# Kernel tuning notes

Hardware: AMD Instinct MI355X
Metric: run time of the kernel (lower is better)

The kernel has to match this reference:

```python
import jax, jax.numpy as jnp
import numpy as np

N_EMB = 1024
HEAD_SIZE = 128

def setup_inputs() -> dict:
    key = jax.random.key(0)
    kx, kq, kk, kv = jax.random.split(key, 4)
    s = 1.0 / np.sqrt(N_EMB)
    return {
        "x": jax.random.normal(kx, (4, 4096, N_EMB), dtype=jnp.float32),
        "Wq": jax.random.normal(kq, (N_EMB, HEAD_SIZE), dtype=jnp.float32) * s,
        "Wk": jax.random.normal(kk, (N_EMB, HEAD_SIZE), dtype=jnp.float32) * s,
        "Wv": jax.random.normal(kv, (N_EMB, HEAD_SIZE), dtype=jnp.float32) * s,
    }

def reference(x, Wq, Wk, Wv) -> jnp.ndarray:
    B, T, C = x.shape
    q = jnp.einsum('btc,cd->btd', x, Wq)  # [B,T,H]
    k = jnp.einsum('btc,cd->btd', x, Wk)
    v = jnp.einsum('btc,cd->btd', x, Wv)
    # NOTE: original scales by sqrt(n_emb), not sqrt(head_size)
    wei = jnp.einsum('btd,bsd->bts', q, k) / jnp.sqrt(jnp.asarray(C, x.dtype))
    causal = jnp.tril(jnp.ones((T, T), dtype=bool))
    wei = jnp.where(causal, wei, -jnp.inf)
    wei = jax.nn.softmax(wei, axis=-1)
    return jnp.einsum('bts,bsd->btd', wei, v)
```

## Files before the change

kernel.cpp:

```cpp
#include <hip/hip_runtime.h>
#include <hip/hip_bf16.h>


#define TSEQ 4096
#define NBATCH 4
#define CEMB 1024
#define HS 128
#define NWORK 272

typedef float  f32x4  __attribute__((ext_vector_type(4)));
typedef float  f32x16 __attribute__((ext_vector_type(16)));
typedef __bf16 bf16x4 __attribute__((ext_vector_type(4)));
typedef __bf16 bf16x8 __attribute__((ext_vector_type(8)));
typedef int    i32x2  __attribute__((ext_vector_type(2)));
typedef int    i32x4  __attribute__((ext_vector_type(4)));

__device__ __forceinline__ __bf16 f2b(float f) { return (__bf16)f; }
__device__ __forceinline__ float fexp2(float f) { return __builtin_amdgcn_exp2f(f); }

__global__ void wtrans_kernel(const float* __restrict__ Wq,
                              const float* __restrict__ Wk,
                              const float* __restrict__ Wv,
                              __bf16* __restrict__ Wt) {
  const float* W = (blockIdx.y == 0) ? Wq : (blockIdx.y == 1) ? Wk : Wv;
  int g  = blockIdx.x * 256 + threadIdx.x;
  int n  = g & 127;
  int k0 = (g >> 7) * 8;
  bf16x8 v;
#pragma unroll
  for (int i = 0; i < 8; ++i) v[i] = f2b(W[(size_t)(k0 + i) * HS + n]);
  *(bf16x8*)(Wt + (size_t)blockIdx.y * HS * CEMB + (size_t)n * CEMB + k0) = v;
}

__global__ __launch_bounds__(128)
void proj_kernel(const float* __restrict__ x, const __bf16* __restrict__ Wt,
                 __bf16* __restrict__ qb, __bf16* __restrict__ kb,
                 __bf16* __restrict__ vt) {
  __shared__ __align__(16) __bf16 As[64 * 72];
  __shared__ __align__(16) __bf16 Bs[128 * 72];

  const int tid  = threadIdx.x;
  const int lane = tid & 63;
  const int w    = tid >> 6;
  const int l31  = lane & 31;
  const int half = lane >> 5;

  const int bid   = blockIdx.x;
  const int xcd   = bid & 7;
  const int rest  = bid >> 3;
  const int mat   = rest % 3;
  const int mslab = rest / 3;
  const int m0    = (xcd + 8 * mslab) * 64;
  const __bf16* Wm = Wt + (size_t)mat * HS * CEMB;

  f32x16 acc[2][2];
#pragma unroll
  for (int a = 0; a < 2; ++a)
#pragma unroll
    for (int b = 0; b < 2; ++b)
#pragma unroll
      for (int r = 0; r < 16; ++r) acc[a][b][r] = 0.f;

  const int srow = tid >> 3;
  const int soff = tid & 7;

  f32x4  pa[4][2];
  bf16x8 pb[8];
#pragma unroll
  for (int i = 0; i < 4; ++i) {
    const float* p = x + (size_t)(m0 + srow + 16 * i) * CEMB + soff * 8;
    pa[i][0] = *(const f32x4*)p;
    pa[i][1] = *(const f32x4*)(p + 4);
  }
#pragma unroll
  for (int i = 0; i < 8; ++i)
    pb[i] = *(const bf16x8*)(Wm + (size_t)(srow + 16 * i) * CEMB + soff * 8);

  for (int ks = 0; ks < CEMB; ks += 64) {
    __syncthreads();
#pragma unroll
    for (int i = 0; i < 4; ++i) {
      bf16x8 h;
#pragma unroll
      for (int j = 0; j < 4; ++j) {
        h[j]     = f2b(pa[i][0][j]);
        h[4 + j] = f2b(pa[i][1][j]);
      }
      *(bf16x8*)(As + (srow + 16 * i) * 72 + soff * 8) = h;
    }
#pragma unroll
    for (int i = 0; i < 8; ++i)
      *(bf16x8*)(Bs + (srow + 16 * i) * 72 + soff * 8) = pb[i];
    __syncthreads();
    if (ks + 64 < CEMB) {
#pragma unroll
      for (int i = 0; i < 4; ++i) {
        const float* p = x + (size_t)(m0 + srow + 16 * i) * CEMB + ks + 64 + soff * 8;
        pa[i][0] = *(const f32x4*)p;
        pa[i][1] = *(const f32x4*)(p + 4);
      }
#pragma unroll
      for (int i = 0; i < 8; ++i)
        pb[i] = *(const bf16x8*)(Wm + (size_t)(srow + 16 * i) * CEMB + ks + 64 + soff * 8);
    }
#pragma unroll
    for (int kc = 0; kc < 4; ++kc) {
      bf16x8 af[2], bf[2];
#pragma unroll
      for (int mi = 0; mi < 2; ++mi)
        af[mi] = *(const bf16x8*)(As + (mi * 32 + l31) * 72 + kc * 16 + half * 8);
#pragma unroll
      for (int ni = 0; ni < 2; ++ni)
        bf[ni] = *(const bf16x8*)(Bs + (64 * w + ni * 32 + l31) * 72 + kc * 16 + half * 8);
#pragma unroll
      for (int mi = 0; mi < 2; ++mi)
#pragma unroll
        for (int ni = 0; ni < 2; ++ni)
          acc[mi][ni] = __builtin_amdgcn_mfma_f32_32x32x16_bf16(
              af[mi], bf[ni], acc[mi][ni], 0, 0, 0);
    }
  }

  const float qscale = 1.4426950408889634f / 32.0f;
  if (mat == 0) {
#pragma unroll
    for (int mi = 0; mi < 2; ++mi)
#pragma unroll
      for (int ni = 0; ni < 2; ++ni) {
        int n = 64 * w + ni * 32 + l31;
#pragma unroll
        for (int r = 0; r < 16; ++r) {
          int m = m0 + mi * 32 + (r & 3) + 8 * (r >> 2) + 4 * half;
          qb[(size_t)m * HS + n] = f2b(acc[mi][ni][r] * qscale);
        }
      }
  } else if (mat == 1) {
#pragma unroll
    for (int mi = 0; mi < 2; ++mi)
#pragma unroll
      for (int ni = 0; ni < 2; ++ni) {
        int n = 64 * w + ni * 32 + l31;
#pragma unroll
        for (int r = 0; r < 16; ++r) {
          int m = m0 + mi * 32 + (r & 3) + 8 * (r >> 2) + 4 * half;
          kb[(size_t)m * HS + n] = f2b(acc[mi][ni][r]);
        }
      }
  } else {
    const int bt = m0 >> 12;
#pragma unroll
    for (int mi = 0; mi < 2; ++mi)
#pragma unroll
      for (int ni = 0; ni < 2; ++ni) {
        int n = 64 * w + ni * 32 + l31;
#pragma unroll
        for (int g = 0; g < 4; ++g) {
          bf16x4 pk;
#pragma unroll
          for (int d = 0; d < 4; ++d) pk[d] = f2b(acc[mi][ni][4 * g + d]);
          int tl = ((m0 + mi * 32) & 4095) + 8 * g + 4 * half;
          *(bf16x4*)(vt + ((size_t)bt * HS + n) * TSEQ + tl) = pk;
        }
      }
  }
}

__global__ __launch_bounds__(256)
void attn_kernel(const __bf16* __restrict__ qb, const __bf16* __restrict__ kb,
                 const __bf16* __restrict__ vt,
                 __bf16* __restrict__ Opart, float* __restrict__ Lpart) {
  __shared__ __align__(16) __bf16 Kt[64 * 136];
  __shared__ __align__(16) __bf16 Vtl[128 * 72];

  const int tid   = threadIdx.x;
  const int lane  = tid & 63;
  const int w     = tid >> 6;
  const int l31   = lane & 31;
  const int half  = lane >> 5;
  const int batch = blockIdx.y;
  const int xw    = blockIdx.x;

  int q = 0;
  while (q < 31 && xw >= (((q + 2) * (q + 2)) >> 2)) ++q;
  const int split = xw - (((q + 1) * (q + 1)) >> 2);
  const int ntile = 2 * (q + 1);
  const int nsp   = (q + 2) >> 1;
  const int tps   = (ntile + nsp - 1) / nsp;
  const int it0   = split * tps;
  const int it1   = min(it0 + tps, ntile);

  const int strip0 = q * 128 + w * 32;
  const size_t bbase = (size_t)batch * TSEQ;

  bf16x8 qf[8];
  {
    const __bf16* qr = qb + (bbase + strip0 + l31) * HS + half * 8;
#pragma unroll
    for (int kc = 0; kc < 8; ++kc) qf[kc] = *(const bf16x8*)(qr + kc * 16);
  }

  const __bf16* kbb = kb + bbase * HS;
  const __bf16* vbb = vt + (size_t)batch * HS * TSEQ;

  bf16x8 pkr[4], pvr[4];
  {
    const int c0 = it0 * 64;
#pragma unroll
    for (int i = 0; i < 4; ++i) {
      int c = tid + i * 256;
      pkr[i] = *(const bf16x8*)(kbb + (size_t)(c0 + (c >> 4)) * HS + (c & 15) * 8);
      pvr[i] = *(const bf16x8*)(vbb + (size_t)(c >> 3) * TSEQ + c0 + (c & 7) * 8);
    }
  }

  f32x16 o[4];
#pragma unroll
  for (int nt = 0; nt < 4; ++nt)
#pragma unroll
    for (int r = 0; r < 16; ++r) o[nt][r] = 0.f;
  float lsum = 0.f;

  for (int it = it0; it < it1; ++it) {
    const int c0 = it * 64;
    __syncthreads();
#pragma unroll
    for (int i = 0; i < 4; ++i) {
      int c = tid + i * 256;
      *(bf16x8*)(&Kt[(c >> 4) * 136 + (c & 15) * 8]) = pkr[i];
      *(bf16x8*)(&Vtl[(c >> 3) * 72 + (c & 7) * 8]) = pvr[i];
    }
    __syncthreads();
    if (it + 1 < it1) {
      const int c1 = c0 + 64;
#pragma unroll
      for (int i = 0; i < 4; ++i) {
        int c = tid + i * 256;
        pkr[i] = *(const bf16x8*)(kbb + (size_t)(c1 + (c >> 4)) * HS + (c & 15) * 8);
        pvr[i] = *(const bf16x8*)(vbb + (size_t)(c >> 3) * TSEQ + c1 + (c & 7) * 8);
      }
    }

    if (c0 <= strip0 + 31) {
      i32x2 pkt[2][4];
#pragma unroll
      for (int t = 0; t < 2; ++t)
#pragma unroll
        for (int j = 0; j < 4; ++j) pkt[t][j] = (i32x2){0, 0};

#pragma unroll
      for (int t = 0; t < 2; ++t) {
        if (c0 + t * 32 <= strip0 + 31) {
          f32x16 s;
#pragma unroll
          for (int r = 0; r < 16; ++r) s[r] = 0.f;
          __builtin_amdgcn_s_setprio(1);
#pragma unroll
          for (int kc = 0; kc < 8; ++kc) {
            bf16x8 kf = *(const bf16x8*)(&Kt[(t * 32 + l31) * 136 + kc * 16 + half * 8]);
            s = __builtin_amdgcn_mfma_f32_32x32x16_bf16(kf, qf[kc], s, 0, 0, 0);
          }
          __builtin_amdgcn_s_setprio(0);
          if (c0 + t * 32 + 31 > strip0) {
#pragma unroll
            for (int r = 0; r < 16; ++r) {
              int key = c0 + t * 32 + (r & 3) + 8 * (r >> 2) + 4 * half;
              if (key > strip0 + l31) s[r] = -INFINITY;
            }
          }
          float p[16], ps = 0.f;
#pragma unroll
          for (int r = 0; r < 16; ++r) { p[r] = fexp2(s[r]); ps += p[r]; }
          lsum += ps;
#pragma unroll
          for (int j = 0; j < 4; ++j) {
            bf16x4 t4;
#pragma unroll
            for (int d = 0; d < 4; ++d) t4[d] = f2b(p[4 * j + d]);
            pkt[t][j] = __builtin_bit_cast(i32x2, t4);
          }
        }
      }
#pragma unroll
      for (int kk = 0; kk < 4; ++kk) {
        int t = kk >> 1, lo = (kk & 1) * 2;
        i32x2 a = pkt[t][lo], b = pkt[t][lo + 1];
        i32x4 af4;
#if defined(__has_builtin) && __has_builtin(__builtin_amdgcn_permlane32_swap)
        {
          auto r0 = __builtin_amdgcn_permlane32_swap(a.x, b.x, false, false);
          auto r1 = __builtin_amdgcn_permlane32_swap(a.y, b.y, false, false);
          af4.x = r0[0]; af4.y = r1[0]; af4.z = r0[1]; af4.w = r1[1];
        }
#else
        {
          i32x2 ra, rb;
          ra.x = __shfl_xor(a.x, 32); ra.y = __shfl_xor(a.y, 32);
          rb.x = __shfl_xor(b.x, 32); rb.y = __shfl_xor(b.y, 32);
          af4.x = half ? rb.x : a.x;
          af4.y = half ? rb.y : a.y;
          af4.z = half ? b.x  : ra.x;
          af4.w = half ? b.y  : ra.y;
        }
#endif
        bf16x8 af = __builtin_bit_cast(bf16x8, af4);
        __builtin_amdgcn_s_setprio(1);
#pragma unroll
        for (int nt = 0; nt < 4; ++nt) {
          bf16x8 vf = *(const bf16x8*)(&Vtl[(nt * 32 + l31) * 72 + kk * 16 + half * 8]);
          o[nt] = __builtin_amdgcn_mfma_f32_32x32x16_bf16(af, vf, o[nt], 0, 0, 0);
        }
        __builtin_amdgcn_s_setprio(0);
      }
    }
  }

  const size_t widx = (size_t)batch * NWORK + xw;
  __bf16* Op = Opart + widx * (128 * 128);
#pragma unroll
  for (int r = 0; r < 16; ++r) {
    int rloc = w * 32 + 4 * half + (r & 3) + 8 * (r >> 2);
#pragma unroll
    for (int nt = 0; nt < 4; ++nt)
      Op[rloc * 128 + nt * 32 + l31] = f2b(o[nt][r]);
  }
  lsum += __shfl_xor(lsum, 32);
  if (half == 0) Lpart[widx * 128 + w * 32 + l31] = lsum;
}

__global__ __launch_bounds__(256)
void reduce_kernel(const __bf16* __restrict__ Opart, const float* __restrict__ Lpart,
                   float* __restrict__ out) {
  const int batch = blockIdx.y;
  const int rowg  = blockIdx.x * 8 + (threadIdx.x >> 5);
  const int q = rowg >> 7;
  const int nsp = (q + 2) >> 1;
  const int off = ((q + 1) * (q + 1)) >> 2;
  const size_t wbase = (size_t)batch * NWORK + off;
  const int row128 = rowg & 127;
  const int c0 = (threadIdx.x & 31) * 4;

  float l = 0.f;
  for (int s = 0; s < nsp; ++s) l += Lpart[(wbase + s) * 128 + row128];
  const float inv = 1.0f / l;

  const __bf16* op = Opart + wbase * (128 * 128) + row128 * 128 + c0;
  f32x4 a = {0.f, 0.f, 0.f, 0.f};
  for (int s = 0; s < nsp; ++s) {
    bf16x4 v = *(const bf16x4*)(op + (size_t)s * 128 * 128);
#pragma unroll
    for (int j = 0; j < 4; ++j) a[j] += (float)v[j];
  }
  a *= inv;
  *(f32x4*)(out + ((size_t)batch * TSEQ + rowg) * HS + c0) = a;
}

extern "C" void kernel_launch(void* const* d_in, const int* in_sizes, int n_in,
                              void* d_out, int out_size, void* d_ws, size_t ws_size,
                              hipStream_t stream) {
  const float* x  = (const float*)d_in[0];
  const float* Wq = (const float*)d_in[1];
  const float* Wk = (const float*)d_in[2];
  const float* Wv = (const float*)d_in[3];
  float* out = (float*)d_out;

  char* ws = (char*)d_ws;
  __bf16* Wt = (__bf16*)ws;
  __bf16* qb = (__bf16*)(ws + 786432);
  __bf16* kb = (__bf16*)(ws + 786432 + 4194304);
  __bf16* vt = (__bf16*)(ws + 786432 + 2 * 4194304);
  __bf16* Opart = (__bf16*)(ws + 786432 + 3 * 4194304);
  float*  Lpart = (float*)(ws + 786432 + 3 * 4194304 +
                           (size_t)NBATCH * NWORK * 128 * 128 * 2);

  wtrans_kernel<<<dim3(64, 3), 256, 0, stream>>>(Wq, Wk, Wv, Wt);
  proj_kernel<<<dim3(768), 128, 0, stream>>>(x, Wt, qb, kb, vt);
  attn_kernel<<<dim3(NWORK, NBATCH), 256, 0, stream>>>(qb, kb, vt, Opart, Lpart);
  reduce_kernel<<<dim3(512, NBATCH), 256, 0, stream>>>(Opart, Lpart, out);
}
```

Measured before the change: 180.3 us.

## Double-buffer K/V tiles in LDS via direct global-to-LDS loads with XOR swizzle

Replaces register-staged K/V prefetch (global→VGPR→LDS with two barriers) with direct global_load_lds into double-buffered LDS tiles, so only one barrier per iteration is needed. Padding is replaced by an XOR swizzle on 16-byte chunks to avoid bank conflicts, and the reads apply the same swizzle. This frees registers and overlaps the next tile's load with compute. It doubles LDS use, which may lower occupancy, and the vmcnt(0) wait at the loop top may expose load latency.

```diff
diff --git a/kernel.cpp b/kernel.cpp
--- a/kernel.cpp
+++ b/kernel.cpp
@@ -17,6 +17,12 @@
 
 __device__ __forceinline__ __bf16 f2b(float f) { return (__bf16)f; }
 __device__ __forceinline__ float fexp2(float f) { return __builtin_amdgcn_exp2f(f); }
+
+typedef const __attribute__((address_space(1))) void* gas_ptr;
+typedef __attribute__((address_space(3))) void* las_ptr;
+__device__ __forceinline__ void gload16(const void* g, void* l) {
+  __builtin_amdgcn_global_load_lds((gas_ptr)g, (las_ptr)l, 16, 0, 0);
+}
 
 __global__ void wtrans_kernel(const float* __restrict__ Wq,
                               const float* __restrict__ Wk,
@@ -169,8 +175,8 @@
 void attn_kernel(const __bf16* __restrict__ qb, const __bf16* __restrict__ kb,
                  const __bf16* __restrict__ vt,
                  __bf16* __restrict__ Opart, float* __restrict__ Lpart) {
-  __shared__ __align__(16) __bf16 Kt[64 * 136];
-  __shared__ __align__(16) __bf16 Vtl[128 * 72];
+  __shared__ __align__(16) __bf16 Kt[2][64 * 128];
+  __shared__ __align__(16) __bf16 Vt[2][128 * 64];
 
   const int tid   = threadIdx.x;
   const int lane  = tid & 63;
@@ -202,16 +208,20 @@
   const __bf16* kbb = kb + bbase * HS;
   const __bf16* vbb = vt + (size_t)batch * HS * TSEQ;
 
-  bf16x8 pkr[4], pvr[4];
-  {
-    const int c0 = it0 * 64;
+  auto stage = [&](int buf, int c0) {
 #pragma unroll
     for (int i = 0; i < 4; ++i) {
-      int c = tid + i * 256;
-      pkr[i] = *(const bf16x8*)(kbb + (size_t)(c0 + (c >> 4)) * HS + (c & 15) * 8);
-      pvr[i] = *(const bf16x8*)(vbb + (size_t)(c >> 3) * TSEQ + c0 + (c & 7) * 8);
-    }
-  }
+      int idx  = w * 256 + i * 64 + lane;
+      int krow = idx >> 4;
+      int kug  = (idx & 15) ^ (krow & 7);
+      gload16(kbb + (size_t)(c0 + krow) * HS + kug * 8,
+              &Kt[buf][(w * 256 + i * 64) * 8]);
+      int d   = idx >> 3;
+      int vug = (idx & 7) ^ (d & 7);
+      gload16(vbb + (size_t)d * TSEQ + c0 + vug * 8,
+              &Vt[buf][(w * 256 + i * 64) * 8]);
+    }
+  };
 
   f32x16 o[4];
 #pragma unroll
@@ -220,25 +230,14 @@
     for (int r = 0; r < 16; ++r) o[nt][r] = 0.f;
   float lsum = 0.f;
 
+  int cur = 0;
+  stage(0, it0 * 64);
+
   for (int it = it0; it < it1; ++it) {
     const int c0 = it * 64;
+    asm volatile("s_waitcnt vmcnt(0)" ::: "memory");
     __syncthreads();
-#pragma unroll
-    for (int i = 0; i < 4; ++i) {
-      int c = tid + i * 256;
-      *(bf16x8*)(&Kt[(c >> 4) * 136 + (c & 15) * 8]) = pkr[i];
-      *(bf16x8*)(&Vtl[(c >> 3) * 72 + (c & 7) * 8]) = pvr[i];
-    }
-    __syncthreads();
-    if (it + 1 < it1) {
-      const int c1 = c0 + 64;
-#pragma unroll
-      for (int i = 0; i < 4; ++i) {
-        int c = tid + i * 256;
-        pkr[i] = *(const bf16x8*)(kbb + (size_t)(c1 + (c >> 4)) * HS + (c & 15) * 8);
-        pvr[i] = *(const bf16x8*)(vbb + (size_t)(c >> 3) * TSEQ + c1 + (c & 7) * 8);
-      }
-    }
+    if (it + 1 < it1) stage(cur ^ 1, c0 + 64);
 
     if (c0 <= strip0 + 31) {
       i32x2 pkt[2][4];
@@ -256,7 +255,9 @@
           __builtin_amdgcn_s_setprio(1);
 #pragma unroll
           for (int kc = 0; kc < 8; ++kc) {
-            bf16x8 kf = *(const bf16x8*)(&Kt[(t * 32 + l31) * 136 + kc * 16 + half * 8]);
+            int u = 2 * kc + half;
+            bf16x8 kf = *(const bf16x8*)(
+                &Kt[cur][(t * 32 + l31) * 128 + ((u ^ (l31 & 7)) * 8)]);
             s = __builtin_amdgcn_mfma_f32_32x32x16_bf16(kf, qf[kc], s, 0, 0, 0);
           }
           __builtin_amdgcn_s_setprio(0);
@@ -306,12 +307,15 @@
         __builtin_amdgcn_s_setprio(1);
 #pragma unroll
         for (int nt = 0; nt < 4; ++nt) {
-          bf16x8 vf = *(const bf16x8*)(&Vtl[(nt * 32 + l31) * 72 + kk * 16 + half * 8]);
+          int u = 2 * kk + half;
+          bf16x8 vf = *(const bf16x8*)(
+              &Vt[cur][(nt * 32 + l31) * 64 + ((u ^ (l31 & 7)) * 8)]);
           o[nt] = __builtin_amdgcn_mfma_f32_32x32x16_bf16(af, vf, o[nt], 0, 0, 0);
         }
         __builtin_amdgcn_s_setprio(0);
       }
     }
+    cur ^= 1;
   }
 
   const size_t widx = (size_t)batch * NWORK + xw;
```

Measured after the change: 168.6 us. 6.5% less time.
